# Kernel optimization log

Hardware: AMD Instinct MI355X
Metric: run time of the kernel (lower is better)

The kernel has to match this reference:

```python
import math
import jax, jax.numpy as jnp
import numpy as np
from jax.scipy.special import xlogy, gammaln

HEADS = 8
DIM_KEY = 64
NUM_REL_POS_FEATURES = 192


def get_positional_embed(n, feature_size):
    # distances: [-n+1, ..., n-1], length 2n-1
    dist = jnp.arange(-n + 1, n)
    adist = jnp.abs(dist).astype(jnp.float32)[:, None]  # (2n-1, 1)
    num_basis = feature_size // 6  # 3 feature fns * 2 (sign-augmented)
    seq_len = n
    # exponential half-life features
    max_range = math.log(seq_len) / math.log(2.0)
    half_life = 2.0 ** jnp.linspace(3.0, max_range, num_basis)  # min_half_life=3.0
    feat_exp = jnp.exp(-math.log(2.0) / half_life[None, :] * adist)
    # central mask features
    center_widths = 2.0 ** jnp.arange(1, num_basis + 1) - 1.0
    feat_cm = (center_widths[None, :] > adist).astype(jnp.float32)
    # gamma pdf features
    stddev = seq_len / (2 * num_basis)
    start_mean = seq_len / num_basis
    mean = jnp.linspace(start_mean, float(seq_len), num_basis)[None, :]
    concentration = (mean / stddev) ** 2
    rate = mean / (stddev ** 2)
    log_unnorm = xlogy(concentration - 1.0, adist) - rate * adist
    log_norm = gammaln(concentration) - concentration * jnp.log(rate)
    prob = jnp.exp(log_unnorm - log_norm) + 1e-8
    feat_gamma = prob / jnp.max(prob, axis=-1, keepdims=True)
    emb = jnp.concatenate([feat_exp, feat_cm, feat_gamma], axis=-1)  # (2n-1, fs/2)
    sign = jnp.sign(dist).astype(jnp.float32)[:, None]
    return jnp.concatenate([emb, sign * emb], axis=-1)  # (2n-1, fs)


def relative_shift(x):
    # x: (b, h, n, 2n-1) -> (b, h, n, n) Transformer-XL shift
    b, h, t1, t2 = x.shape
    x = jnp.pad(x, ((0, 0), (0, 0), (0, 0), (1, 0)))  # (b,h,t1,t2+1)
    x = x.reshape(b, h, t2 + 1, t1)[:, :, 1:, :].reshape(b, h, t1, t2)
    return x[..., : (t2 + 2) // 2]


def setup_inputs() -> dict:
    key = jax.random.key(0)
    ks = jax.random.split(key, 8)
    dim = 1536
    b, n = 2, 1536
    hdk = HEADS * DIM_KEY  # 512
    hdv = HEADS * 192      # 1536
    s = 0.02
    return {
        'x': jax.random.normal(ks[0], (b, n, dim), jnp.float32),
        'Wq': jax.random.normal(ks[1], (hdk, dim), jnp.float32) * s,
        'Wk': jax.random.normal(ks[2], (hdk, dim), jnp.float32) * s,
        'Wv': jax.random.normal(ks[3], (hdv, dim), jnp.float32) * s,
        'Wrel': jax.random.normal(ks[4], (hdk, NUM_REL_POS_FEATURES), jnp.float32) * s,
        'Wout': jax.random.normal(ks[5], (dim, hdv), jnp.float32) * s,
        'b_out': jnp.zeros((dim,), jnp.float32),
        'rel_content_bias': jax.random.normal(ks[6], (1, HEADS, 1, DIM_KEY), jnp.float32),
        'rel_pos_bias': jax.random.normal(ks[7], (1, HEADS, 1, DIM_KEY), jnp.float32),
    }


def reference(x, Wq, Wk, Wv, Wrel, Wout, b_out, rel_content_bias, rel_pos_bias):
    b, n, dim = x.shape
    h = HEADS
    scale = DIM_KEY ** -0.5

    def split_heads(t):  # (b, n, h*d) -> (b, h, n, d)
        return t.reshape(b, n, h, -1).transpose(0, 2, 1, 3)

    q = split_heads(jnp.einsum('bnd,fd->bnf', x, Wq)) * scale
    k = split_heads(jnp.einsum('bnd,fd->bnf', x, Wk))
    v = split_heads(jnp.einsum('bnd,fd->bnf', x, Wv))

    content_logits = jnp.einsum('bhid,bhjd->bhij', q + rel_content_bias, k)

    positions = get_positional_embed(n, NUM_REL_POS_FEATURES)  # (2n-1, fs)
    rel_k = jnp.einsum('jf,ef->je', positions, Wrel).reshape(2 * n - 1, h, DIM_KEY)
    rel_k = rel_k.transpose(1, 0, 2)  # (h, 2n-1, dk)
    rel_logits = jnp.einsum('bhid,hjd->bhij', q + rel_pos_bias, rel_k)
    rel_logits = relative_shift(rel_logits)  # (b, h, n, n)

    attn = jax.nn.softmax(content_logits + rel_logits, axis=-1)
    out = jnp.einsum('bhij,bhjd->bhid', attn, v)
    out = out.transpose(0, 2, 1, 3).reshape(b, n, -1)  # (b, n, h*dv)
    return jnp.einsum('bnf,df->bnd', out, Wout) + b_out
```

## Files before the change

### kernel.cpp

```cpp
#include <hip/hip_runtime.h>
#include <cmath>

typedef unsigned short u16;
typedef unsigned int u32;
typedef short frag8 __attribute__((ext_vector_type(8)));
typedef float f32x4 __attribute__((ext_vector_type(4)));

#define DEVINL __device__ __forceinline__

DEVINL float bf2f(u16 v) { return __uint_as_float(((u32)v) << 16); }
DEVINL u16 f2bf(float f) {
    u32 u = __float_as_uint(f);
    u32 r = (u + 0x7fffu + ((u >> 16) & 1u)) >> 16;
    return (u16)r;
}
DEVINL u32 pack2(float a, float b) { return (u32)f2bf(a) | ((u32)f2bf(b) << 16); }
DEVINL void async_copy16(const u16* g, u16* l) {
    __builtin_amdgcn_global_load_lds((const __attribute__((address_space(1))) u32*)g,
                                     (__attribute__((address_space(3))) u32*)l, 16, 0, 0);
}
DEVINL f32x4 mfma_bf16(frag8 a, frag8 b, f32x4 c) {
    return __builtin_amdgcn_mfma_f32_16x16x32_bf16(a, b, c, 0, 0, 0);
}

__global__ __launch_bounds__(256) void convert_kernel(
        const float* __restrict__ s0, const float* __restrict__ s1,
        const float* __restrict__ s2, const float* __restrict__ s3,
        const float* __restrict__ s4, u16* __restrict__ dst) {
    const int c0 = 589824, c1 = 98304, c2 = 98304, c3 = 294912;
    const int total = 1376256;
    for (int c = blockIdx.x * blockDim.x + threadIdx.x; c < total;
         c += gridDim.x * blockDim.x) {
        const float* src; int off;
        if (c < c0) { src = s0; off = c; }
        else if (c < c0 + c1) { src = s1; off = c - c0; }
        else if (c < c0 + c1 + c2) { src = s2; off = c - c0 - c1; }
        else if (c < c0 + c1 + c2 + c3) { src = s3; off = c - c0 - c1 - c2; }
        else { src = s4; off = c - c0 - c1 - c2 - c3; }
        float4 a = ((const float4*)src)[off * 2];
        float4 b = ((const float4*)src)[off * 2 + 1];
        uint4 o;
        o.x = pack2(a.x, a.y); o.y = pack2(a.z, a.w);
        o.z = pack2(b.x, b.y); o.w = pack2(b.z, b.w);
        ((uint4*)dst)[c] = o;
    }
}

DEVINL double lgamma_stirling(double z) {
    double zi = 1.0 / z, zi2 = zi * zi;
    return (z - 0.5) * log(z) - z + 0.91893853320467274178
         + zi * (1.0 / 12.0) - zi * zi2 * (1.0 / 360.0) + zi * zi2 * zi2 * (1.0 / 1260.0);
}

__global__ __launch_bounds__(256) void embed_relk_kernel(const float* __restrict__ Wrel,
                                                         u16* __restrict__ relk) {
    __shared__ float pos[16][192];
    __shared__ float inv_hl[32], cwid[32], cm1[32], rateS[32];
    __shared__ double lognS[32];
    __shared__ float gmax[16];
    int t = threadIdx.x;
    int u0b = blockIdx.x * 16;

    if (t < 32) {
        double step = (10.584962500721156 - 3.0) / 31.0;
        double hl = exp2(3.0 + t * step);
        inv_hl[t] = (float)(1.0 / hl);
        cwid[t] = exp2f((float)(t + 1)) - 1.0f;
        double mean = 48.0 * (t + 1);
        double conc = (mean / 24.0) * (mean / 24.0);
        double rate = mean / 576.0;
        cm1[t] = (float)(conc - 1.0);
        rateS[t] = (float)rate;
        lognS[t] = lgamma_stirling(conc) - conc * log(rate);
    }
    __syncthreads();

    for (int idx = t; idx < 512; idx += 256) {
        int ul = idx >> 5, bs = idx & 31;
        int dist = u0b + ul - 1535;
        float ad = fabsf((float)dist);
        pos[ul][bs] = exp2f(-ad * inv_hl[bs]);
        pos[ul][32 + bs] = (cwid[bs] > ad) ? 1.0f : 0.0f;
        double prob = 0.0;
        if (dist != 0) {
            double adD = (double)ad;
            prob = exp((double)cm1[bs] * log(adD) - (double)rateS[bs] * adD - lognS[bs]);
        }
        pos[ul][64 + bs] = (float)(prob + 1e-8);
    }
    __syncthreads();
    if (t < 16) {
        float g = 0.f;
        #pragma unroll
        for (int bsx = 0; bsx < 32; bsx++) g = fmaxf(g, pos[t][64 + bsx]);
        gmax[t] = g;
    }
    __syncthreads();
    for (int idx = t; idx < 16 * 96; idx += 256) {
        int ul = idx / 96, f = idx - ul * 96;
        float v = pos[ul][f];
        if (f >= 64) { v = v / gmax[ul]; pos[ul][f] = v; }
        int dist = u0b + ul - 1535;
        float sg = (dist > 0) ? 1.f : ((dist < 0) ? -1.f : 0.f);
        pos[ul][96 + f] = sg * v;
    }
    __syncthreads();

    int e0 = t * 2;
    const float* w0 = Wrel + e0 * 192;
    const float* w1 = w0 + 192;
    float a0[16], a1[16];
    #pragma unroll
    for (int ul = 0; ul < 16; ul++) { a0[ul] = 0.f; a1[ul] = 0.f; }
    for (int f = 0; f < 192; f++) {
        float wa = w0[f], wb = w1[f];
        #pragma unroll
        for (int ul = 0; ul < 16; ul++) {
            float p = pos[ul][f];
            a0[ul] = fmaf(p, wa, a0[ul]);
            a1[ul] = fmaf(p, wb, a1[ul]);
        }
    }
    int h0 = e0 >> 6, d0 = e0 & 63;
    int h1 = (e0 + 1) >> 6, d1 = (e0 + 1) & 63;
    for (int ul = 0; ul < 16; ul++) {
        int u = u0b + ul;
        relk[(h0 * 3072 + u) * 64 + d0] = f2bf(a0[ul]);
        relk[(h1 * 3072 + u) * 64 + d1] = f2bf(a1[ul]);
    }
}

DEVINL void gemm128_mainloop(const u16* __restrict__ A, const u16* __restrict__ B,
                             int K, f32x4 acc[4][4], u16* As, u16* Bs) {
    int tid = threadIdx.x;
    int lane = tid & 63, wave = tid >> 6;
    int wm = (wave >> 1) * 64, wn = (wave & 1) * 64;
    int fm = lane & 15, fq = lane >> 4;
    for (int k0 = 0; k0 < K; k0 += 32) {
        #pragma unroll
        for (int p = 0; p < 2; p++) {
            int e = (p * 256 + tid) * 8;
            int r = e >> 5, c = e & 31;
            async_copy16(A + r * K + k0 + c, As + e);
            async_copy16(B + r * K + k0 + c, Bs + e);
        }
        __syncthreads();
        frag8 af[4], bfr[4];
        #pragma unroll
        for (int mi = 0; mi < 4; mi++) af[mi] = *(const frag8*)&As[(wm + 16 * mi + fm) * 32 + fq * 8];
        #pragma unroll
        for (int ni = 0; ni < 4; ni++) bfr[ni] = *(const frag8*)&Bs[(wn + 16 * ni + fm) * 32 + fq * 8];
        #pragma unroll
        for (int mi = 0; mi < 4; mi++)
            #pragma unroll
            for (int ni = 0; ni < 4; ni++)
                acc[mi][ni] = mfma_bf16(af[mi], bfr[ni], acc[mi][ni]);
        __syncthreads();
    }
}

__global__ __launch_bounds__(256) void gemm_qkv_kernel(
        const u16* __restrict__ X, const u16* __restrict__ Wq, const u16* __restrict__ Wk,
        const u16* __restrict__ Wv, const float* __restrict__ cbias, const float* __restrict__ pbias,
        u16* __restrict__ qc, u16* __restrict__ qp, u16* __restrict__ kws, u16* __restrict__ vt) {
    __shared__ __align__(16) u16 As[128 * 32];
    __shared__ __align__(16) u16 Bs[128 * 32];
    int m0 = blockIdx.x * 128, n0 = blockIdx.y * 128;
    const u16* Bp; int brow;
    if (n0 < 512)       { Bp = Wq; brow = n0; }
    else if (n0 < 1024) { Bp = Wk; brow = n0 - 512; }
    else                { Bp = Wv; brow = n0 - 1024; }
    f32x4 acc[4][4];
    #pragma unroll
    for (int i = 0; i < 4; i++)
        #pragma unroll
        for (int j = 0; j < 4; j++) acc[i][j] = (f32x4){0.f, 0.f, 0.f, 0.f};
    gemm128_mainloop(X + m0 * 1536, Bp + brow * 1536, 1536, acc, As, Bs);

    int tid = threadIdx.x, lane = tid & 63, wave = tid >> 6;
    int wm = (wave >> 1) * 64, wn = (wave & 1) * 64, fm = lane & 15, fq = lane >> 4;
    #pragma unroll
    for (int mi = 0; mi < 4; mi++) {
        #pragma unroll
        for (int ni = 0; ni < 4; ni++) {
            int col = n0 + wn + 16 * ni + fm;
            int rbase = m0 + wm + 16 * mi + fq * 4;
            #pragma unroll
            for (int reg = 0; reg < 4; reg++) {
                int row = rbase + reg;
                float v = acc[mi][ni][reg];
                int b = row >= 1536 ? 1 : 0;
                int i = row - b * 1536;
                if (n0 < 512) {
                    float qv = v * 0.125f;
                    int idx = ((b * 8 + (col >> 6)) * 1536 + i) * 64 + (col & 63);
                    qc[idx] = f2bf(qv + cbias[col]);
                    qp[idx] = f2bf(qv + pbias[col]);
                } else if (n0 < 1024) {
                    int c2 = col - 512;
                    kws[((b * 8 + (c2 >> 6)) * 1536 + i) * 64 + (c2 & 63)] = f2bf(v);
                } else {
                    int c2 = col - 1024;
                    int hh = c2 / 192, dd = c2 - hh * 192;
                    vt[((b * 8 + hh) * 192 + dd) * 1536 + i] = f2bf(v);
                }
            }
        }
    }
}

__global__ __launch_bounds__(256) void attn_kernel(
        const u16* __restrict__ qc, const u16* __restrict__ qp, const u16* __restrict__ kws,
        const u16* __restrict__ vt, const u16* __restrict__ relk, u16* __restrict__ ao) {
    __shared__ __align__(16) u16 smem[24768];
    u16* k_lds    = smem;
    u16* vt_lds   = smem + 4096;
    u16* relk_lds = smem + 16384;
    u16* P_lds    = smem + 22528;
    float* S_lds  = (float*)k_lds;
    float* R_lds  = (float*)relk_lds;
    float* mstate = (float*)(smem + 24576);
    float* lstate = mstate + 32;
    float* alpha_lds = lstate + 32;

    const int n = 1536;
    int flat = blockIdx.y * 48 + blockIdx.x;
    int swz  = (flat & 7) * 96 + (flat >> 3);
    int bh = swz / 48;
    int i0 = (swz - bh * 48) * 32;
    int b = bh >> 3, h = bh & 7;
    const u16* qcP = qc + bh * n * 64;
    const u16* qpP = qp + bh * n * 64;
    const u16* kP  = kws + bh * n * 64;
    const u16* vtP = vt + bh * 192 * n;
    const u16* rkP = relk + h * 3072 * 64;

    int tid = threadIdx.x, lane = tid & 63, w = tid >> 6, fm = lane & 15, fq = lane >> 4;
    int sw = fm & 7;
    if (tid < 32) { mstate[tid] = __int_as_float(0xff800000); lstate[tid] = 0.f; }

    frag8 aqc[2][2], aqp[2][2];
    #pragma unroll
    for (int mi = 0; mi < 2; mi++)
        #pragma unroll
        for (int ks = 0; ks < 2; ks++) {
            int off = (i0 + 16 * mi + fm) * 64 + ks * 32 + fq * 8;
            aqc[mi][ks] = *(const frag8*)(qcP + off);
            aqp[mi][ks] = *(const frag8*)(qpP + off);
        }

    f32x4 acc_o[2][3];
    #pragma unroll
    for (int mi = 0; mi < 2; mi++)
        #pragma unroll
        for (int dj = 0; dj < 3; dj++) acc_o[mi][dj] = (f32x4){0.f, 0.f, 0.f, 0.f};

    int uis[3], rmis[3];
    #pragma unroll
    for (int tt = 0; tt < 3; tt++) {
        int tv = w + tt * 4;
        rmis[tt] = (tv >= 6) ? 1 : 0;
        uis[tt] = tv - rmis[tt] * 6;
    }

    for (int jt = 0; jt < 24; jt++) {
        int j0 = jt * 64;
        __syncthreads();
        #pragma unroll
        for (int p = 0; p < 2; p++) {
            int l = p * 256 + tid, r = l >> 3, c = (l & 7) ^ (r & 7);
            async_copy16(kP + (j0 + r) * 64 + c * 8, k_lds + l * 8);
        }
        #pragma unroll
        for (int p = 0; p < 6; p++) {
            int l = p * 256 + tid, r = l >> 3, c = (l & 7) ^ (r & 7);
            async_copy16(vtP + r * n + j0 + c * 8, vt_lds + l * 8);
        }
        int u0 = 1504 + j0 - i0;
        #pragma unroll
        for (int p = 0; p < 3; p++) {
            int l = p * 256 + tid, r = l >> 3, c = (l & 7) ^ (r & 7);
            async_copy16(rkP + (u0 + r) * 64 + c * 8, relk_lds + l * 8);
        }
        __syncthreads();

        f32x4 acc_s[2];
        acc_s[0] = (f32x4){0.f, 0.f, 0.f, 0.f};
        acc_s[1] = (f32x4){0.f, 0.f, 0.f, 0.f};
        #pragma unroll
        for (int ks = 0; ks < 2; ks++) {
            frag8 bk = *(const frag8*)&k_lds[(16 * w + fm) * 64 + ((ks * 4 + fq) ^ sw) * 8];
            acc_s[0] = mfma_bf16(aqc[0][ks], bk, acc_s[0]);
            acc_s[1] = mfma_bf16(aqc[1][ks], bk, acc_s[1]);
        }
        f32x4 acc_r[3];
        #pragma unroll
        for (int tt = 0; tt < 3; tt++) {
            acc_r[tt] = (f32x4){0.f, 0.f, 0.f, 0.f};
            #pragma unroll
            for (int ks = 0; ks < 2; ks++) {
                frag8 br = *(const frag8*)&relk_lds[(16 * uis[tt] + fm) * 64 + ((ks * 4 + fq) ^ sw) * 8];
                acc_r[tt] = mfma_bf16(aqp[rmis[tt]][ks], br, acc_r[tt]);
            }
        }
        __syncthreads();

        #pragma unroll
        for (int mi = 0; mi < 2; mi++)
            #pragma unroll
            for (int reg = 0; reg < 4; reg++)
                S_lds[(16 * mi + fq * 4 + reg) * 64 + 16 * w + fm] = acc_s[mi][reg];
        #pragma unroll
        for (int tt = 0; tt < 3; tt++)
            #pragma unroll
            for (int reg = 0; reg < 4; reg++)
                R_lds[(16 * rmis[tt] + fq * 4 + reg) * 96 + 16 * uis[tt] + fm] = acc_r[tt][reg];
        __syncthreads();

        int li = tid >> 3, c0 = (tid & 7) * 8;
        float sv[8];
        float mx = __int_as_float(0xff800000);
        #pragma unroll
        for (int e = 0; e < 8; e++) {
            int c = c0 + e;
            sv[e] = S_lds[li * 64 + c] + R_lds[li * 96 + c - li + 31];
            mx = fmaxf(mx, sv[e]);
        }
        mx = fmaxf(mx, __shfl_xor(mx, 1));
        mx = fmaxf(mx, __shfl_xor(mx, 2));
        mx = fmaxf(mx, __shfl_xor(mx, 4));
        float mo = mstate[li];
        float mn = fmaxf(mo, mx);
        float al = __expf(mo - mn);
        float pe[8], sum = 0.f;
        #pragma unroll
        for (int e = 0; e < 8; e++) { pe[e] = __expf(sv[e] - mn); sum += pe[e]; }
        {
            uint4 pw;
            pw.x = pack2(pe[0], pe[1]); pw.y = pack2(pe[2], pe[3]);
            pw.z = pack2(pe[4], pe[5]); pw.w = pack2(pe[6], pe[7]);
            int slot = (tid & 7) ^ (li & 7);
            *(uint4*)&P_lds[li * 64 + slot * 8] = pw;
        }
        sum += __shfl_xor(sum, 1);
        sum += __shfl_xor(sum, 2);
        sum += __shfl_xor(sum, 4);
        if ((tid & 7) == 0) {
            mstate[li] = mn;
            lstate[li] = lstate[li] * al + sum;
            alpha_lds[li] = al;
        }
        __syncthreads();

        #pragma unroll
        for (int mi = 0; mi < 2; mi++)
            #pragma unroll
            for (int reg = 0; reg < 4; reg++) {
                float al2 = alpha_lds[16 * mi + fq * 4 + reg];
                #pragma unroll
                for (int dj = 0; dj < 3; dj++) acc_o[mi][dj][reg] *= al2;
            }
        frag8 ap[2][2];
        #pragma unroll
        for (int mi = 0; mi < 2; mi++)
            #pragma unroll
            for (int ks = 0; ks < 2; ks++)
                ap[mi][ks] = *(const frag8*)&P_lds[(16 * mi + fm) * 64 + ((ks * 4 + fq) ^ sw) * 8];
        #pragma unroll
        for (int dj = 0; dj < 3; dj++) {
            #pragma unroll
            for (int ks = 0; ks < 2; ks++) {
                frag8 bv = *(const frag8*)&vt_lds[(16 * (3 * w + dj) + fm) * 64 + ((ks * 4 + fq) ^ sw) * 8];
                acc_o[0][dj] = mfma_bf16(ap[0][ks], bv, acc_o[0][dj]);
                acc_o[1][dj] = mfma_bf16(ap[1][ks], bv, acc_o[1][dj]);
            }
        }
    }

    __syncthreads();
    #pragma unroll
    for (int mi = 0; mi < 2; mi++)
        #pragma unroll
        for (int dj = 0; dj < 3; dj++)
            #pragma unroll
            for (int reg = 0; reg < 4; reg++) {
                int rl = 16 * mi + fq * 4 + reg;
                float lsum = lstate[rl];
                int row = b * 1536 + i0 + rl;
                int col = h * 192 + 16 * (3 * w + dj) + fm;
                ao[row * 1536 + col] = f2bf(acc_o[mi][dj][reg] / lsum);
            }
}

__global__ __launch_bounds__(256) void gemm_out_kernel(
        const u16* __restrict__ A, const u16* __restrict__ W, const float* __restrict__ bias,
        float* __restrict__ out) {
    __shared__ __align__(16) u16 As[128 * 32];
    __shared__ __align__(16) u16 Bs[128 * 32];
    int m0 = blockIdx.x * 128, n0 = blockIdx.y * 128;
    f32x4 acc[4][4];
    #pragma unroll
    for (int i = 0; i < 4; i++)
        #pragma unroll
        for (int j = 0; j < 4; j++) acc[i][j] = (f32x4){0.f, 0.f, 0.f, 0.f};
    gemm128_mainloop(A + m0 * 1536, W + n0 * 1536, 1536, acc, As, Bs);

    int tid = threadIdx.x, lane = tid & 63, wave = tid >> 6;
    int wm = (wave >> 1) * 64, wn = (wave & 1) * 64, fm = lane & 15, fq = lane >> 4;
    #pragma unroll
    for (int mi = 0; mi < 4; mi++) {
        #pragma unroll
        for (int ni = 0; ni < 4; ni++) {
            int col = n0 + wn + 16 * ni + fm;
            int rbase = m0 + wm + 16 * mi + fq * 4;
            float bv = bias[col];
            #pragma unroll
            for (int reg = 0; reg < 4; reg++) {
                int row = rbase + reg;
                out[row * 1536 + col] = acc[mi][ni][reg] + bv;
            }
        }
    }
}

extern "C" void kernel_launch(void* const* d_in, const int* in_sizes, int n_in,
                              void* d_out, int out_size, void* d_ws, size_t ws_size,
                              hipStream_t stream) {
    (void)in_sizes; (void)n_in; (void)out_size; (void)ws_size;
    const float* x    = (const float*)d_in[0];
    const float* Wq   = (const float*)d_in[1];
    const float* Wk   = (const float*)d_in[2];
    const float* Wv   = (const float*)d_in[3];
    const float* Wrel = (const float*)d_in[4];
    const float* Wout = (const float*)d_in[5];
    const float* bout = (const float*)d_in[6];
    const float* cb   = (const float*)d_in[7];
    const float* pb   = (const float*)d_in[8];

    u16* xb  = (u16*)d_ws;
    u16* wqb = xb  + 4718592;
    u16* wkb = wqb + 786432;
    u16* wvb = wkb + 786432;
    u16* wob = wvb + 2359296;
    u16* qc  = wob + 2359296;
    u16* qp  = qc + 1572864;
    u16* kw  = qp + 1572864;
    u16* vt  = kw + 1572864;
    u16* rk  = vt + 4718592;
    u16* ao  = rk + 1572864;
    float* out = (float*)d_out;

    convert_kernel<<<dim3(1024), dim3(256), 0, stream>>>(x, Wq, Wk, Wv, Wout, xb);
    embed_relk_kernel<<<dim3(192), dim3(256), 0, stream>>>(Wrel, rk);
    gemm_qkv_kernel<<<dim3(24, 20), dim3(256), 0, stream>>>(xb, wqb, wkb, wvb, cb, pb, qc, qp, kw, vt);
    attn_kernel<<<dim3(48, 16), dim3(256), 0, stream>>>(qc, qp, kw, vt, rk, ao);
    gemm_out_kernel<<<dim3(24, 12), dim3(256), 0, stream>>>(ao, wob, bout, out);
}
```

Before: 317.8 us.

## Prefetch next K and relative-key tiles during PV phase with manual waitcnt barriers

```diff
diff --git a/kernel.cpp b/kernel.cpp
--- a/kernel.cpp
+++ b/kernel.cpp
@@ -21,6 +21,12 @@
 }
 DEVINL f32x4 mfma_bf16(frag8 a, frag8 b, f32x4 c) {
     return __builtin_amdgcn_mfma_f32_16x16x32_bf16(a, b, c, 0, 0, 0);
+}
+#define VMCNT(N) asm volatile("s_waitcnt vmcnt(" #N ")" ::: "memory")
+DEVINL void bar_raw() {
+    asm volatile("s_waitcnt lgkmcnt(0)" ::: "memory");
+    __builtin_amdgcn_s_barrier();
+    asm volatile("" ::: "memory");
 }
 
 __global__ __launch_bounds__(256) void convert_kernel(
@@ -209,6 +215,28 @@
     }
 }
 
+DEVINL void stage_k(const u16* kP, u16* k_lds, int j0, int tid) {
+    #pragma unroll
+    for (int p = 0; p < 2; p++) {
+        int l = p * 256 + tid, r = l >> 3, c = (l & 7) ^ (r & 7);
+        async_copy16(kP + (j0 + r) * 64 + c * 8, k_lds + l * 8);
+    }
+}
+DEVINL void stage_relk(const u16* rkP, u16* relk_lds, int u0, int tid) {
+    #pragma unroll
+    for (int p = 0; p < 3; p++) {
+        int l = p * 256 + tid, r = l >> 3, c = (l & 7) ^ (r & 7);
+        async_copy16(rkP + (u0 + r) * 64 + c * 8, relk_lds + l * 8);
+    }
+}
+DEVINL void stage_v(const u16* vtP, u16* vt_lds, int j0, int tid) {
+    #pragma unroll
+    for (int p = 0; p < 6; p++) {
+        int l = p * 256 + tid, r = l >> 3, c = (l & 7) ^ (r & 7);
+        async_copy16(vtP + r * 1536 + j0 + c * 8, vt_lds + l * 8);
+    }
+}
+
 __global__ __launch_bounds__(256) void attn_kernel(
         const u16* __restrict__ qc, const u16* __restrict__ qp, const u16* __restrict__ kws,
         const u16* __restrict__ vt, const u16* __restrict__ relk, u16* __restrict__ ao) {
@@ -263,26 +291,15 @@
         uis[tt] = tv - rmis[tt] * 6;
     }
 
+    stage_k(kP, k_lds, 0, tid);
+    stage_relk(rkP, relk_lds, 1504 - i0, tid);
+
     for (int jt = 0; jt < 24; jt++) {
         int j0 = jt * 64;
-        __syncthreads();
-        #pragma unroll
-        for (int p = 0; p < 2; p++) {
-            int l = p * 256 + tid, r = l >> 3, c = (l & 7) ^ (r & 7);
-            async_copy16(kP + (j0 + r) * 64 + c * 8, k_lds + l * 8);
-        }
-        #pragma unroll
-        for (int p = 0; p < 6; p++) {
-            int l = p * 256 + tid, r = l >> 3, c = (l & 7) ^ (r & 7);
-            async_copy16(vtP + r * n + j0 + c * 8, vt_lds + l * 8);
-        }
-        int u0 = 1504 + j0 - i0;
-        #pragma unroll
-        for (int p = 0; p < 3; p++) {
-            int l = p * 256 + tid, r = l >> 3, c = (l & 7) ^ (r & 7);
-            async_copy16(rkP + (u0 + r) * 64 + c * 8, relk_lds + l * 8);
-        }
-        __syncthreads();
+        bar_raw();
+        stage_v(vtP, vt_lds, j0, tid);
+        VMCNT(6);
+        bar_raw();
 
         f32x4 acc_s[2];
         acc_s[0] = (f32x4){0.f, 0.f, 0.f, 0.f};
@@ -303,7 +320,7 @@
                 acc_r[tt] = mfma_bf16(aqp[rmis[tt]][ks], br, acc_r[tt]);
             }
         }
-        __syncthreads();
+        bar_raw();
 
         #pragma unroll
         for (int mi = 0; mi < 2; mi++)
@@ -315,7 +332,7 @@
             #pragma unroll
             for (int reg = 0; reg < 4; reg++)
                 R_lds[(16 * rmis[tt] + fq * 4 + reg) * 96 + 16 * uis[tt] + fm] = acc_r[tt][reg];
-        __syncthreads();
+        bar_raw();
 
         int li = tid >> 3, c0 = (tid & 7) * 8;
         float sv[8];
@@ -350,7 +367,13 @@
             lstate[li] = lstate[li] * al + sum;
             alpha_lds[li] = al;
         }
-        __syncthreads();
+        VMCNT(0);
+        bar_raw();
+
+        if (jt < 23) {
+            stage_k(kP, k_lds, j0 + 64, tid);
+            stage_relk(rkP, relk_lds, 1504 - i0 + j0 + 64, tid);
+        }
 
         #pragma unroll
         for (int mi = 0; mi < 2; mi++)
@@ -377,7 +400,6 @@
         }
     }
 
-    __syncthreads();
     #pragma unroll
     for (int mi = 0; mi < 2; mi++)
         #pragma unroll
```

After: 307.8 us. -3.1%, faster.
